# Kernel tuning notes

Measured on AMD Instinct MI355X. Metric: run time of the kernel, lower is better.

## Reference

```python
import jax, jax.numpy as jnp
import numpy as np

N_NODES = 50000
N_EDGES = 500000
D_IN = 128
D_HID = 128
C = 1.0          # curvature (same for every layer)
MIN_NORM = 1e-15
MAX_TANH_ARG = 15.0
PROJ_EPS = 4e-3  # float32 boundary eps used by hgcn PoincareBall.proj


def _artanh(x):
    x = jnp.clip(x, -1.0 + 1e-7, 1.0 - 1e-7)
    return 0.5 * (jnp.log1p(x) - jnp.log1p(-x))


def _tanh(x):
    return jnp.tanh(jnp.clip(x, -MAX_TANH_ARG, MAX_TANH_ARG))


def _norm(x):
    return jnp.maximum(jnp.linalg.norm(x, axis=-1, keepdims=True), MIN_NORM)


def proj(x, c):
    # clip points to stay strictly inside the Poincare ball
    n = _norm(x)
    maxnorm = (1.0 - PROJ_EPS) / jnp.sqrt(c)
    return jnp.where(n > maxnorm, x / n * maxnorm, x)


def expmap0(u, c):
    sc = jnp.sqrt(c)
    n = _norm(u)
    return _tanh(sc * n) * u / (sc * n)


def logmap0(p, c):
    sc = jnp.sqrt(c)
    n = _norm(p)
    return _artanh(sc * n) * p / (sc * n)


def mobius_add(x, y, c):
    x2 = jnp.sum(x * x, -1, keepdims=True)
    y2 = jnp.sum(y * y, -1, keepdims=True)
    xy = jnp.sum(x * y, -1, keepdims=True)
    num = (1.0 + 2.0 * c * xy + c * y2) * x + (1.0 - c * x2) * y
    den = 1.0 + 2.0 * c * xy + c * c * x2 * y2
    return num / jnp.maximum(den, MIN_NORM)


def mobius_matvec(m, x, c):
    sc = jnp.sqrt(c)
    xn = _norm(x)
    mx = x @ m.T                                   # [N, out]
    mxn = _norm(mx)
    res = _tanh(mxn / xn * _artanh(sc * xn)) * mx / (mxn * sc)
    is_zero = jnp.all(mx == 0.0, axis=-1, keepdims=True)
    return jnp.where(is_zero, jnp.zeros_like(res), res)


def hyp_linear(x, W, b, c):
    h = proj(mobius_matvec(W, x, c), c)
    hyp_bias = proj(expmap0(b[None, :], c), c)     # proj_tan0 is identity on the ball
    return proj(mobius_add(h, hyp_bias, c), c)


def hyp_agg(x, src, dst, edge_weight, c):
    x_tan = logmap0(x, c)                          # [N, d] tangent at origin
    msg = edge_weight[:, None] * x_tan[src]        # [E, d] gather + scale
    agg = jax.ops.segment_sum(msg, dst, num_segments=N_NODES)  # spmm(adj, x_tan)
    return proj(expmap0(agg, c), c)


def hyp_act(x, c_in, c_out):
    xt = jax.nn.relu(logmap0(x, c_in))
    return proj(expmap0(xt, c_out), c_out)


def setup_inputs() -> dict:
    key = jax.random.key(0)
    ks = jax.random.split(key, 8)
    x = jax.random.normal(ks[0], (N_NODES, D_IN), dtype=jnp.float32) * 0.1
    src = jax.random.randint(ks[1], (N_EDGES,), 0, N_NODES)
    dst = jax.random.randint(ks[2], (N_EDGES,), 0, N_NODES)
    edge_weight = jax.random.uniform(ks[3], (N_EDGES,), dtype=jnp.float32) * 0.1
    s1 = 1.0 / np.sqrt(D_IN)
    W1 = jax.random.normal(ks[4], (D_HID, D_IN), dtype=jnp.float32) * s1
    b1 = jax.random.normal(ks[5], (D_HID,), dtype=jnp.float32) * 0.01
    W2 = jax.random.normal(ks[6], (D_HID, D_HID), dtype=jnp.float32) * s1
    b2 = jax.random.normal(ks[7], (D_HID,), dtype=jnp.float32) * 0.01
    return {"x": x, "src": src, "dst": dst, "edge_weight": edge_weight,
            "W1": W1, "b1": b1, "W2": W2, "b2": b2}


def reference(x, src, dst, edge_weight, W1, b1, W2, b2):
    c = jnp.float32(C)
    # HGCN.encode: proj_tan0 (identity for PoincareBall) -> expmap0 -> proj
    h = proj(expmap0(x, c), c)
    # layer 1: HypLinear -> HypAgg -> HypAct
    h = hyp_linear(h, W1, b1, c)
    h = hyp_agg(h, src, dst, edge_weight, c)
    h = hyp_act(h, c, c)
    # layer 2
    h = hyp_linear(h, W2, b2, c)
    h = hyp_agg(h, src, dst, edge_weight, c)
    h = hyp_act(h, c, c)
    return h
```

## Files before the change

### kernel.cpp

```cpp
#include <hip/hip_runtime.h>
#include <math.h>

#define MIN_NORM 1e-15f
#define MAXNORM  0.996f
#define ARTANH_CLIP 0.99999988f

typedef __bf16 bf16x8 __attribute__((ext_vector_type(8)));
typedef float  f32x4  __attribute__((ext_vector_type(4)));

union FragU { ushort u[8]; uint4 q; bf16x8 v; };

__device__ __forceinline__ float wave_sum(float v) {
#pragma unroll
    for (int off = 32; off > 0; off >>= 1) v += __shfl_xor(v, off, 64);
    return v;
}

__device__ __forceinline__ float tanh_fast(float x) {
    const float t = __expf(2.f * fminf(x, 15.f));
    return 1.f - 2.f / (t + 1.f);
}
__device__ __forceinline__ float artanh_fast(float x) {
    x = fminf(x, ARTANH_CLIP);
    return 0.5f * __logf((1.f + x) / (1.f - x));
}

__device__ __forceinline__ float proj_factor(float n2) {
    float n = fmaxf(sqrtf(n2), MIN_NORM);
    return (n > MAXNORM) ? (MAXNORM / n) : 1.f;
}

__device__ __forceinline__ unsigned short f2bf(float f) {
    unsigned u = __float_as_uint(f);
    return (unsigned short)((u + 0x7fffu + ((u >> 16) & 1u)) >> 16);
}
__device__ __forceinline__ float bf2f(unsigned short h) {
    return __uint_as_float((unsigned)h << 16);
}
__device__ __forceinline__ float bflo(unsigned u) { return __uint_as_float(u << 16); }
__device__ __forceinline__ float bfhi(unsigned u) { return __uint_as_float(u & 0xffff0000u); }

__device__ __forceinline__ void red16_f4(float4& v) {
#pragma unroll
    for (int off = 1; off < 16; off <<= 1) {
        v.x += __shfl_xor(v.x, off, 64);
        v.y += __shfl_xor(v.y, off, 64);
        v.z += __shfl_xor(v.z, off, 64);
        v.w += __shfl_xor(v.w, off, 64);
    }
}

__device__ __forceinline__ float bcast_row(const float4& v, int r) {
    const int src = (r >> 2) << 4;
    const float a = __shfl(v.x, src, 64);
    const float b = __shfl(v.y, src, 64);
    const float c = __shfl(v.z, src, 64);
    const float d = __shfl(v.w, src, 64);
    const float lo = (r & 1) ? b : a;
    const float hi = (r & 1) ? d : c;
    return (r & 2) ? hi : lo;
}

__device__ __forceinline__ void pack_w4(const float4 w4, int o, int k, char* out) {
    ushort4 h, l;
    h.x = f2bf(w4.x); l.x = f2bf(w4.x - bf2f(h.x));
    h.y = f2bf(w4.y); l.y = f2bf(w4.y - bf2f(h.y));
    h.z = f2bf(w4.z); l.z = f2bf(w4.z - bf2f(h.z));
    h.w = f2bf(w4.w); l.w = f2bf(w4.w - bf2f(h.w));
    const int prow = ((o & 7) << 4) | (o >> 3);
    const unsigned byte = (unsigned)((prow << 8) + (k << 1)) ^ (unsigned)((prow & 7) << 4);
    *reinterpret_cast<ushort4*>(out + byte) = h;
    *reinterpret_cast<ushort4*>(out + 32768 + byte) = l;
}

__global__ void zero_cnt(int* __restrict__ cnt, int N) {
    const int i = blockIdx.x * blockDim.x + threadIdx.x;
    if (i < N) cnt[i] = 0;
}

__global__ __launch_bounds__(256)
void setup_kernel(const float* __restrict__ W1, const float* __restrict__ W2,
                  char* __restrict__ g1, char* __restrict__ g2,
                  const float* __restrict__ b1, const float* __restrict__ b2,
                  float* __restrict__ hb1, float* __restrict__ hb2,
                  const int* __restrict__ dst, int* __restrict__ cnt, int E) {
    const int b = blockIdx.x;
    if (b < 32) {
        const float* W = (b < 16) ? W1 : W2;
        char* out = (b < 16) ? g1 : g2;
        const int i = (((b & 15) * 256) + threadIdx.x) * 4;
        pack_w4(*reinterpret_cast<const float4*>(&W[i]), i >> 7, i & 127, out);
    } else if (b == 32) {
        if (threadIdx.x < 64) {
            const int lane = threadIdx.x;
#pragma unroll
            for (int j = 0; j < 2; ++j) {
                const float* bb = j ? b2 : b1;
                float* hb = j ? hb2 : hb1;
                float v0 = bb[lane], v1 = bb[lane + 64];
                float n2 = wave_sum(v0 * v0 + v1 * v1);
                float n = fmaxf(sqrtf(n2), MIN_NORM);
                float sc = tanh_fast(n) / n;
                sc *= proj_factor(sc * sc * n2);
                hb[lane] = v0 * sc;
                hb[lane + 64] = v1 * sc;
            }
        }
    } else {
        const int e = (b - 33) * 256 + threadIdx.x;
        if (e < E) atomicAdd(&cnt[dst[e]], 1);
    }
}


__global__ void scan1(const int* __restrict__ cnt, int* __restrict__ ptr,
                      int* __restrict__ bsum, int N) {
    __shared__ int s[256];
    const int t = threadIdx.x;
    const int i = blockIdx.x * 256 + t;
    int v = (i < N) ? ((cnt[i] + 3) & ~3) : 0;
    s[t] = v;
    __syncthreads();
#pragma unroll
    for (int off = 1; off < 256; off <<= 1) {
        int add = (t >= off) ? s[t - off] : 0;
        __syncthreads();
        s[t] += add;
        __syncthreads();
    }
    if (i < N) ptr[i] = s[t] - v;
    if (t == 255) bsum[blockIdx.x] = s[255];
}

__global__ void scan2(const int* __restrict__ bsum, int* __restrict__ bscan, int nb) {
    __shared__ int s[256];
    const int t = threadIdx.x;
    int v = (t < nb) ? bsum[t] : 0;
    s[t] = v;
    __syncthreads();
#pragma unroll
    for (int off = 1; off < 256; off <<= 1) {
        int add = (t >= off) ? s[t - off] : 0;
        __syncthreads();
        s[t] += add;
        __syncthreads();
    }
    bscan[t] = s[t] - v;
    if (t == 255) bscan[256] = s[255];
}

__global__ void scan3(const int* __restrict__ bscan, const int* __restrict__ cnt,
                      int* __restrict__ ptr, int* __restrict__ cursor,
                      unsigned* __restrict__ epk, int N) {
    const int i = blockIdx.x * blockDim.x + threadIdx.x;
    if (i < N) {
        const int p = ptr[i] + bscan[i >> 8];
        ptr[i] = p;
        cursor[i] = p;
        const int c = cnt[i];
        const int pc = (c + 3) & ~3;
        for (int j = c; j < pc; ++j) epk[p + j] = 0u;
    }
    if (i == 0) {
        const int tot = bscan[256];
        ptr[N] = tot;
#pragma unroll
        for (int j = 0; j < 16; ++j) epk[tot + j] = 0u;
    }
}

__global__ void scatter_kernel(const int* __restrict__ src, const int* __restrict__ dst,
                               const float* __restrict__ ew, int* __restrict__ cursor,
                               unsigned* __restrict__ epk, int E) {
    int e = blockIdx.x * blockDim.x + threadIdx.x;
    if (e >= E) return;
    int pos = atomicAdd(&cursor[dst[e]], 1);
    epk[pos] = ((unsigned)src[e] << 16) | (unsigned)f2bf(ew[e]);
}

template <bool PRELUDE, bool BF16IN, bool BF16OUT>
__global__ __launch_bounds__(512, 4)
void hyp_linear_tan_mfma(const void* __restrict__ xin, const char* __restrict__ gWpack,
                         const float* __restrict__ hb, void* __restrict__ xtan,
                         int n_rows) {
    __shared__ __align__(16) char sW[65536];

    const int tid = threadIdx.x;
    const int lane = tid & 63, wid = tid >> 6;
    const int r15 = lane & 15, g = lane >> 4;

    const int tiles = (n_rows + 15) >> 4;
    const int tile = blockIdx.x * 8 + wid;
    const bool active = (tile < tiles);
    const int rowbase = tile << 4;
    const int myrow = rowbase + r15;
    const bool rok = active && (myrow < n_rows);

    float4 xa[4], xb[4];
    uint4 xu[4];
    if (BF16IN) {
        const char* xr = (const char*)xin + (size_t)myrow * 256 + g * 16;
#pragma unroll
        for (int kc = 0; kc < 4; ++kc)
            xu[kc] = rok ? *reinterpret_cast<const uint4*>(xr + kc * 64)
                         : make_uint4(0u, 0u, 0u, 0u);
    } else {
        const float* xr = (const float*)xin + (size_t)myrow * 128 + g * 8;
#pragma unroll
        for (int kc = 0; kc < 4; ++kc) {
            if (rok) {
                xa[kc] = *reinterpret_cast<const float4*>(xr + kc * 32);
                xb[kc] = *reinterpret_cast<const float4*>(xr + kc * 32 + 4);
            } else {
                xa[kc] = make_float4(0.f, 0.f, 0.f, 0.f);
                xb[kc] = xa[kc];
            }
        }
    }

    {
        const uint4* gsrc = reinterpret_cast<const uint4*>(gWpack);
        uint4* ldst = reinterpret_cast<uint4*>(sW);
#pragma unroll
        for (int i = 0; i < 8; ++i) ldst[tid + i * 512] = gsrc[tid + i * 512];
    }

    float yb[8];
    {
        const float4 yba = *reinterpret_cast<const float4*>(&hb[r15 * 8]);
        const float4 ybb = *reinterpret_cast<const float4*>(&hb[r15 * 8 + 4]);
        yb[0] = yba.x; yb[1] = yba.y; yb[2] = yba.z; yb[3] = yba.w;
        yb[4] = ybb.x; yb[5] = ybb.y; yb[6] = ybb.z; yb[7] = ybb.w;
    }
    float y2p = 0.f;
#pragma unroll
    for (int t = 0; t < 8; ++t) y2p += yb[t] * yb[t];
#pragma unroll
    for (int off = 1; off < 16; off <<= 1) y2p += __shfl_xor(y2p, off, 64);
    const float y2 = y2p;

    __syncthreads();
    if (!active) return;

    bf16x8 ah[4], al[4];
    float ss = 0.f;
    if (BF16IN) {
#pragma unroll
        for (int kc = 0; kc < 4; ++kc) {
            FragU fu; fu.q = xu[kc];
            ah[kc] = fu.v;
            const uint4 u = xu[kc];
            float f0 = bflo(u.x), f1 = bfhi(u.x), f2_ = bflo(u.y), f3 = bfhi(u.y);
            float f4 = bflo(u.z), f5 = bfhi(u.z), f6 = bflo(u.w), f7 = bfhi(u.w);
            ss += f0 * f0 + f1 * f1 + f2_ * f2_ + f3 * f3
                + f4 * f4 + f5 * f5 + f6 * f6 + f7 * f7;
        }
    } else {
#pragma unroll
        for (int kc = 0; kc < 4; ++kc) {
            const float4 a = xa[kc], b = xb[kc];
            ss += a.x * a.x + a.y * a.y + a.z * a.z + a.w * a.w
                + b.x * b.x + b.y * b.y + b.z * b.z + b.w * b.w;
            ah[kc][0] = (__bf16)a.x; al[kc][0] = (__bf16)(a.x - (float)ah[kc][0]);
            ah[kc][1] = (__bf16)a.y; al[kc][1] = (__bf16)(a.y - (float)ah[kc][1]);
            ah[kc][2] = (__bf16)a.z; al[kc][2] = (__bf16)(a.z - (float)ah[kc][2]);
            ah[kc][3] = (__bf16)a.w; al[kc][3] = (__bf16)(a.w - (float)ah[kc][3]);
            ah[kc][4] = (__bf16)b.x; al[kc][4] = (__bf16)(b.x - (float)ah[kc][4]);
            ah[kc][5] = (__bf16)b.y; al[kc][5] = (__bf16)(b.y - (float)ah[kc][5]);
            ah[kc][6] = (__bf16)b.z; al[kc][6] = (__bf16)(b.z - (float)ah[kc][6]);
            ah[kc][7] = (__bf16)b.w; al[kc][7] = (__bf16)(b.w - (float)ah[kc][7]);
        }
    }
    ss += __shfl_xor(ss, 16, 64);
    ss += __shfl_xor(ss, 32, 64);

    f32x4 acc[8];
#pragma unroll
    for (int ct = 0; ct < 8; ++ct) acc[ct] = (f32x4){0.f, 0.f, 0.f, 0.f};

    const unsigned lswz = (unsigned)((r15 & 7) << 4);
#pragma unroll
    for (int kc = 0; kc < 4; ++kc) {
#pragma unroll
        for (int ct = 0; ct < 8; ++ct) {
            const unsigned byte =
                ((unsigned)((ct << 12) + (r15 << 8) + (kc << 6) + (g << 4))) ^ lswz;
            FragU bh, bl;
            bh.q = *reinterpret_cast<const uint4*>(sW + byte);
            bl.q = *reinterpret_cast<const uint4*>(sW + 32768 + byte);
            acc[ct] = __builtin_amdgcn_mfma_f32_16x16x32_bf16(ah[kc], bh.v, acc[ct], 0, 0, 0);
            acc[ct] = __builtin_amdgcn_mfma_f32_16x16x32_bf16(ah[kc], bl.v, acc[ct], 0, 0, 0);
            if (!BF16IN)
                acc[ct] = __builtin_amdgcn_mfma_f32_16x16x32_bf16(al[kc], bh.v, acc[ct], 0, 0, 0);
        }
    }

    float4 r2 = make_float4(0.f, 0.f, 0.f, 0.f);
    float4 xyv = make_float4(0.f, 0.f, 0.f, 0.f);
#pragma unroll
    for (int ct = 0; ct < 8; ++ct) {
        r2.x += acc[ct][0] * acc[ct][0];
        r2.y += acc[ct][1] * acc[ct][1];
        r2.z += acc[ct][2] * acc[ct][2];
        r2.w += acc[ct][3] * acc[ct][3];
        xyv.x += acc[ct][0] * yb[ct];
        xyv.y += acc[ct][1] * yb[ct];
        xyv.z += acc[ct][2] * yb[ct];
        xyv.w += acc[ct][3] * yb[ct];
    }
    red16_f4(r2);
    red16_f4(xyv);

    const float rn2 = bcast_row(r2, r15);
    const float xyr = bcast_row(xyv, r15);
    const float n2v = ss;

    const float n = fmaxf(sqrtf(n2v), MIN_NORM);
    float sc = 1.f;
    if (PRELUDE) {
        sc = tanh_fast(n) / n;
        sc *= proj_factor(sc * sc * n2v);
    }
    const float xn = fmaxf(sc * n, MIN_NORM);
    const float mxn = fmaxf(sc * sqrtf(rn2), MIN_NORM);
    const float s = tanh_fast(mxn / xn * artanh_fast(xn));
    const float sl0 = (s * sc) / mxn;
    float m2 = rn2 * sl0 * sl0;
    const float f = proj_factor(m2);
    const float scl = sl0 * f;
    m2 *= f * f;
    const float xy = scl * xyr;
    const float cx = 1.f + 2.f * xy + y2;
    const float cy = 1.f - m2;
    const float rdn = 1.f / fmaxf(1.f + 2.f * xy + m2 * y2, MIN_NORM);
    const float A = cx * scl * rdn;
    const float B = cy * rdn;
    const float on2 = A * A * rn2 + 2.f * A * B * xyr + B * B * y2;
    const float f2 = proj_factor(on2);
    const float onn = fmaxf(sqrtf(on2) * f2, MIN_NORM);
    const float slg = artanh_fast(onn) / onn;
    const float P = slg * f2 * A;
    const float Q = slg * f2 * B;

#pragma unroll
    for (int reg = 0; reg < 4; ++reg) {
        const float Pr = __shfl(P, 4 * g + reg, 64);
        const float Qr = __shfl(Q, 4 * g + reg, 64);
        const int row = rowbase + 4 * g + reg;
        if (row < n_rows) {
            float v[8];
#pragma unroll
            for (int ct = 0; ct < 8; ++ct)
                v[ct] = fmaf(Pr, acc[ct][reg], Qr * yb[ct]);
            if (BF16OUT) {
                uint4 pk;
                pk.x = (unsigned)f2bf(v[0]) | ((unsigned)f2bf(v[1]) << 16);
                pk.y = (unsigned)f2bf(v[2]) | ((unsigned)f2bf(v[3]) << 16);
                pk.z = (unsigned)f2bf(v[4]) | ((unsigned)f2bf(v[5]) << 16);
                pk.w = (unsigned)f2bf(v[6]) | ((unsigned)f2bf(v[7]) << 16);
                *reinterpret_cast<uint4*>((char*)xtan + (size_t)row * 256 + r15 * 16) = pk;
            } else {
                float* orow = (float*)xtan + (size_t)row * 128 + r15 * 8;
                *reinterpret_cast<float4*>(orow) = make_float4(v[0], v[1], v[2], v[3]);
                *reinterpret_cast<float4*>(orow + 4) = make_float4(v[4], v[5], v[6], v[7]);
            }
        }
    }
}

template <bool BF16OUT>
__global__ __launch_bounds__(256)
void gather_act(const char* __restrict__ xt, const int* __restrict__ ptr,
                const unsigned* __restrict__ epk, void* __restrict__ out, int n_rows) {
    const int v = blockIdx.x * 4 + (threadIdx.x >> 6);
    if (v >= n_rows) return;
    const int lane = threadIdx.x & 63;
    const int q = lane >> 4, t = lane & 15;
    const char* xtl = xt + (t << 4);
    const int beg = ptr[v];
    const int it = (ptr[v + 1] - beg) >> 2;

    float acc[8];
#pragma unroll
    for (int j = 0; j < 8; ++j) acc[j] = 0.f;

    const unsigned* ep = epk + beg + q;
    unsigned p = (it > 0) ? ep[0] : 0u;
    for (int k = 1; k <= it; ++k) {
        const uint4 u = *reinterpret_cast<const uint4*>(xtl + ((p >> 16) << 8));
        const unsigned pn = ep[k * 4];
        const float w = __uint_as_float(p << 16);
        acc[0] = fmaf(w, bflo(u.x), acc[0]);
        acc[1] = fmaf(w, bfhi(u.x), acc[1]);
        acc[2] = fmaf(w, bflo(u.y), acc[2]);
        acc[3] = fmaf(w, bfhi(u.y), acc[3]);
        acc[4] = fmaf(w, bflo(u.z), acc[4]);
        acc[5] = fmaf(w, bfhi(u.z), acc[5]);
        acc[6] = fmaf(w, bflo(u.w), acc[6]);
        acc[7] = fmaf(w, bfhi(u.w), acc[7]);
        p = pn;
    }

#pragma unroll
    for (int j = 0; j < 8; ++j) {
        acc[j] += __shfl_xor(acc[j], 16, 64);
        acc[j] += __shfl_xor(acc[j], 32, 64);
    }

    float s = 0.f;
#pragma unroll
    for (int j = 0; j < 8; ++j) s += acc[j] * acc[j];
#pragma unroll
    for (int off = 1; off < 16; off <<= 1) s += __shfl_xor(s, off, 64);
    const float n2 = s;

    float n = fmaxf(sqrtf(n2), MIN_NORM);
    float sc = tanh_fast(n) / n;
    float hn2 = sc * sc * n2;
    float f = proj_factor(hn2);
    sc *= f; hn2 *= f * f;
    float hn = fmaxf(sqrtf(hn2), MIN_NORM);
    float sl = artanh_fast(hn) / hn;
    const float scl1 = sc * sl;

    float x[8];
    float s2 = 0.f;
#pragma unroll
    for (int j = 0; j < 8; ++j) {
        x[j] = fmaxf(acc[j] * scl1, 0.f);
        s2 += x[j] * x[j];
    }
#pragma unroll
    for (int off = 1; off < 16; off <<= 1) s2 += __shfl_xor(s2, off, 64);
    float nb = fmaxf(sqrtf(s2), MIN_NORM);
    float scb = tanh_fast(nb) / nb;
    scb *= proj_factor(scb * scb * s2);

    const float o0 = x[2 * q] * scb, o1 = x[2 * q + 1] * scb;
    if (BF16OUT) {
        const unsigned pk = (unsigned)f2bf(o0) | ((unsigned)f2bf(o1) << 16);
        *reinterpret_cast<unsigned*>((char*)out + (size_t)v * 256 + t * 16 + q * 4) = pk;
    } else {
        *reinterpret_cast<float2*>((float*)out + (size_t)v * 128 + t * 8 + q * 2) =
            make_float2(o0, o1);
    }
}

__global__ __launch_bounds__(256)
void agg_edges(const float* __restrict__ xtan, const int* __restrict__ src,
               const int* __restrict__ dst, const float* __restrict__ ew,
               float* __restrict__ agg, int n_edges) {
    int gt = blockIdx.x * blockDim.x + threadIdx.x;
    int e = gt >> 5;
    if (e >= n_edges) return;
    int c = (gt & 31) << 2;
    int sN = src[e], dN = dst[e];
    float w = ew[e];
    const float4 v = *reinterpret_cast<const float4*>(&xtan[(size_t)sN * 128 + c]);
    float* ap = &agg[(size_t)dN * 128 + c];
    atomicAdd(ap + 0, w * v.x);
    atomicAdd(ap + 1, w * v.y);
    atomicAdd(ap + 2, w * v.z);
    atomicAdd(ap + 3, w * v.w);
}

__global__ __launch_bounds__(256)
void hyp_act_kernel(const float* __restrict__ in, float* __restrict__ out, int n_rows) {
    int row = blockIdx.x * 4 + (threadIdx.x >> 6);
    if (row >= n_rows) return;
    int lane = threadIdx.x & 63;
    int l2 = lane << 1;
    const float2 v = *reinterpret_cast<const float2*>(&in[(size_t)row * 128 + l2]);
    float a0 = v.x, a1 = v.y;
    float n2 = wave_sum(a0 * a0 + a1 * a1);
    float n = fmaxf(sqrtf(n2), MIN_NORM);
    float sc = tanh_fast(n) / n;
    float hn2 = sc * sc * n2;
    float f = proj_factor(hn2);
    sc *= f; hn2 *= f * f;
    float h0 = a0 * sc, h1 = a1 * sc;
    float hn = fmaxf(sqrtf(hn2), MIN_NORM);
    float sl = artanh_fast(hn) / hn;
    float x0 = fmaxf(h0 * sl, 0.f), x1 = fmaxf(h1 * sl, 0.f);
    float n2b = wave_sum(x0 * x0 + x1 * x1);
    float nb = fmaxf(sqrtf(n2b), MIN_NORM);
    float scb = tanh_fast(nb) / nb;
    scb *= proj_factor(scb * scb * n2b);
    *reinterpret_cast<float2*>(&out[(size_t)row * 128 + l2]) =
        make_float2(x0 * scb, x1 * scb);
}

__global__ void bias_kernel(const float* __restrict__ b1, const float* __restrict__ b2,
                            float* __restrict__ hb1, float* __restrict__ hb2) {
    int lane = threadIdx.x;
#pragma unroll
    for (int j = 0; j < 2; ++j) {
        const float* b = j ? b2 : b1;
        float* hb = j ? hb2 : hb1;
        float v0 = b[lane], v1 = b[lane + 64];
        float n2 = wave_sum(v0 * v0 + v1 * v1);
        float n = fmaxf(sqrtf(n2), MIN_NORM);
        float sc = tanh_fast(n) / n;
        sc *= proj_factor(sc * sc * n2);
        hb[lane] = v0 * sc;
        hb[lane + 64] = v1 * sc;
    }
}

__global__ void prep_w(const float* __restrict__ W1, const float* __restrict__ W2,
                       char* __restrict__ g1, char* __restrict__ g2) {
    const int b = blockIdx.x;
    const float* W = (b < 16) ? W1 : W2;
    char* out = (b < 16) ? g1 : g2;
    const int i = (((b & 15) * 256) + threadIdx.x) * 4;
    pack_w4(*reinterpret_cast<const float4*>(&W[i]), i >> 7, i & 127, out);
}

extern "C" void kernel_launch(void* const* d_in, const int* in_sizes, int n_in,
                              void* d_out, int out_size, void* d_ws, size_t ws_size,
                              hipStream_t stream) {
    const float* x   = (const float*)d_in[0];
    const int*   src = (const int*)d_in[1];
    const int*   dst = (const int*)d_in[2];
    const float* ew  = (const float*)d_in[3];
    const float* W1  = (const float*)d_in[4];
    const float* b1  = (const float*)d_in[5];
    const float* W2  = (const float*)d_in[6];
    const float* b2  = (const float*)d_in[7];

    const int N = in_sizes[0] / 128;
    const int E = in_sizes[1];
    float* fout = (float*)d_out;

    const int tiles = (N + 15) >> 4;
    const int lin_grid = (tiles + 7) / 8;
    const int nbE = (E + 255) / 256;
    const int nbN = (N + 255) / 256;

    const size_t epk_words = (size_t)E + 3 * (size_t)N + 16;

    const size_t need = 131072 + 1024
                      + (size_t)N * 256 * 2
                      + (epk_words + N) * 4
                      + ((size_t)(N + 1) + N) * 4
                      + 4096;

    if (ws_size >= need) {
        char*  base  = (char*)d_ws;
        char*  gW1p  = base;
        char*  gW2p  = base + 65536;
        float* hb1   = (float*)(base + 131072);
        float* hb2   = hb1 + 128;
        char*  xtA   = base + 131072 + 1024;
        char*  xtB   = xtA + (size_t)N * 256;
        unsigned* epk = (unsigned*)(xtB + (size_t)N * 256);
        int* cnt     = (int*)(epk + epk_words);
        int* ptr     = cnt + N;
        int* cursor  = ptr + (N + 1);
        int* bsum    = cursor + N;
        int* bscan   = bsum + 256;

        zero_cnt<<<nbN, 256, 0, stream>>>(cnt, N);
        setup_kernel<<<33 + nbE, 256, 0, stream>>>(W1, W2, gW1p, gW2p,
                                                   b1, b2, hb1, hb2, dst, cnt, E);
        scan1<<<nbN, 256, 0, stream>>>(cnt, ptr, bsum, N);
        scan2<<<1, 256, 0, stream>>>(bsum, bscan, nbN);
        scan3<<<nbN, 256, 0, stream>>>(bscan, cnt, ptr, cursor, epk, N);
        scatter_kernel<<<nbE, 256, 0, stream>>>(src, dst, ew, cursor, epk, E);

        hyp_linear_tan_mfma<true, false, true><<<lin_grid, 512, 0, stream>>>(x, gW1p, hb1, xtA, N);
        gather_act<true><<<(N + 3) / 4, 256, 0, stream>>>(xtA, ptr, epk, xtB, N);
        hyp_linear_tan_mfma<false, true, true><<<lin_grid, 512, 0, stream>>>(xtB, gW2p, hb2, xtA, N);
        gather_act<false><<<(N + 3) / 4, 256, 0, stream>>>(xtA, ptr, epk, fout, N);
    } else {
        char*  gW1p = (char*)d_ws;
        char*  gW2p = gW1p + 65536;
        float* hb1  = (float*)(gW2p + 65536);
        float* hb2  = hb1 + 128;
        float* nbuf = hb2 + 128;
        const size_t node_bytes = (size_t)N * 128 * sizeof(float);
        const int agg_blocks = (int)(((size_t)E * 32 + 255) / 256);
        const int row_blocks = (N + 3) / 4;

        prep_w<<<32, 256, 0, stream>>>(W1, W2, gW1p, gW2p);
        bias_kernel<<<1, 64, 0, stream>>>(b1, b2, hb1, hb2);
        hyp_linear_tan_mfma<true, false, false><<<lin_grid, 512, 0, stream>>>(x, gW1p, hb1, fout, N);
        hipMemsetAsync(nbuf, 0, node_bytes, stream);
        agg_edges<<<agg_blocks, 256, 0, stream>>>(fout, src, dst, ew, nbuf, E);
        hyp_act_kernel<<<row_blocks, 256, 0, stream>>>(nbuf, nbuf, N);
        hyp_linear_tan_mfma<false, false, false><<<lin_grid, 512, 0, stream>>>(nbuf, gW2p, hb2, fout, N);
        hipMemsetAsync(fout, 0, node_bytes, stream);
        agg_edges<<<agg_blocks, 256, 0, stream>>>(fout, src, dst, ew, nbuf, E);
        hyp_act_kernel<<<row_blocks, 256, 0, stream>>>(nbuf, fout, N);
    }
}
```

Measured before the change: 170.3 us.

## Split gather into feature-sliced CSR pass plus separate activation kernel

The fused gather+activation kernel is replaced by a gather_slice kernel in which each block handles one of 8 feature slices (32 bytes per row) across a grid-strided set of nodes, with 8 edges processed in parallel per wave. Its fp32 sums go to a new agg buffer, and a separate act_kernel applies expmap/proj/logmap/relu. CSR padding changes from 4 to 8, and the linear kernel's tile mapping becomes interleaved with a minimum grid of 512. The aim is better cache locality on the gathered slices (each slice of xt is small enough to stay cache-resident) at the cost of an extra fp32 round trip through memory and more launches.

```diff
diff --git a/kernel.cpp b/kernel.cpp
--- a/kernel.cpp
+++ b/kernel.cpp
@@ -118,7 +118,7 @@
     __shared__ int s[256];
     const int t = threadIdx.x;
     const int i = blockIdx.x * 256 + t;
-    int v = (i < N) ? ((cnt[i] + 3) & ~3) : 0;
+    int v = (i < N) ? ((cnt[i] + 7) & ~7) : 0;
     s[t] = v;
     __syncthreads();
 #pragma unroll
@@ -158,7 +158,7 @@
         ptr[i] = p;
         cursor[i] = p;
         const int c = cnt[i];
-        const int pc = (c + 3) & ~3;
+        const int pc = (c + 7) & ~7;
         for (int j = c; j < pc; ++j) epk[p + j] = 0u;
     }
     if (i == 0) {
@@ -182,7 +182,7 @@
 __global__ __launch_bounds__(512, 4)
 void hyp_linear_tan_mfma(const void* __restrict__ xin, const char* __restrict__ gWpack,
                          const float* __restrict__ hb, void* __restrict__ xtan,
-                         int n_rows) {
+                         int n_rows, int ngrid) {
     __shared__ __align__(16) char sW[65536];
 
     const int tid = threadIdx.x;
@@ -190,7 +190,7 @@
     const int r15 = lane & 15, g = lane >> 4;
 
     const int tiles = (n_rows + 15) >> 4;
-    const int tile = blockIdx.x * 8 + wid;
+    const int tile = blockIdx.x + ngrid * wid;
     const bool active = (tile < tiles);
     const int rowbase = tile << 4;
     const int myrow = rowbase + r15;
@@ -368,52 +368,49 @@
     }
 }
 
+__global__ __launch_bounds__(256)
+void gather_slice(const char* __restrict__ xt, const int* __restrict__ ptr,
+                  const unsigned* __restrict__ epk, float* __restrict__ agg,
+                  int n_rows, int ngrp) {
+    const int s = blockIdx.x & 7;
+    const int lane = threadIdx.x & 63;
+    const int e8 = lane >> 3, c = lane & 7;
+    const char* xts = xt + s * 32 + c * 4;
+
+    for (int v = (blockIdx.x >> 3) * 4 + ((int)threadIdx.x >> 6); v < n_rows; v += ngrp * 4) {
+        const int beg = ptr[v];
+        const int it = (ptr[v + 1] - beg) >> 3;
+
+        float a0 = 0.f, a1 = 0.f;
+        const unsigned* ep = epk + beg + e8;
+        unsigned p = (it > 0) ? ep[0] : 0u;
+        for (int k = 1; k <= it; ++k) {
+            const unsigned u = *reinterpret_cast<const unsigned*>(xts + ((p >> 16) << 8));
+            const unsigned pn = ep[k * 8];
+            const float w = __uint_as_float(p << 16);
+            a0 = fmaf(w, bflo(u), a0);
+            a1 = fmaf(w, bfhi(u), a1);
+            p = pn;
+        }
+        a0 += __shfl_xor(a0, 8, 64);  a1 += __shfl_xor(a1, 8, 64);
+        a0 += __shfl_xor(a0, 16, 64); a1 += __shfl_xor(a1, 16, 64);
+        a0 += __shfl_xor(a0, 32, 64); a1 += __shfl_xor(a1, 32, 64);
+        if (e8 == 0)
+            *reinterpret_cast<float2*>(agg + (size_t)v * 128 + s * 16 + c * 2) =
+                make_float2(a0, a1);
+    }
+}
+
 template <bool BF16OUT>
-__global__ __launch_bounds__(256)
-void gather_act(const char* __restrict__ xt, const int* __restrict__ ptr,
-                const unsigned* __restrict__ epk, void* __restrict__ out, int n_rows) {
-    const int v = blockIdx.x * 4 + (threadIdx.x >> 6);
+__global__ __launch_bounds__(1024)
+void act_kernel(const float* __restrict__ agg, void* __restrict__ out, int n_rows) {
+    const int v = blockIdx.x * 16 + ((int)threadIdx.x >> 6);
     if (v >= n_rows) return;
-    const int lane = threadIdx.x & 63;
-    const int q = lane >> 4, t = lane & 15;
-    const char* xtl = xt + (t << 4);
-    const int beg = ptr[v];
-    const int it = (ptr[v + 1] - beg) >> 2;
-
-    float acc[8];
-#pragma unroll
-    for (int j = 0; j < 8; ++j) acc[j] = 0.f;
-
-    const unsigned* ep = epk + beg + q;
-    unsigned p = (it > 0) ? ep[0] : 0u;
-    for (int k = 1; k <= it; ++k) {
-        const uint4 u = *reinterpret_cast<const uint4*>(xtl + ((p >> 16) << 8));
-        const unsigned pn = ep[k * 4];
-        const float w = __uint_as_float(p << 16);
-        acc[0] = fmaf(w, bflo(u.x), acc[0]);
-        acc[1] = fmaf(w, bfhi(u.x), acc[1]);
-        acc[2] = fmaf(w, bflo(u.y), acc[2]);
-        acc[3] = fmaf(w, bfhi(u.y), acc[3]);
-        acc[4] = fmaf(w, bflo(u.z), acc[4]);
-        acc[5] = fmaf(w, bfhi(u.z), acc[5]);
-        acc[6] = fmaf(w, bflo(u.w), acc[6]);
-        acc[7] = fmaf(w, bfhi(u.w), acc[7]);
-        p = pn;
-    }
-
-#pragma unroll
-    for (int j = 0; j < 8; ++j) {
-        acc[j] += __shfl_xor(acc[j], 16, 64);
-        acc[j] += __shfl_xor(acc[j], 32, 64);
-    }
-
-    float s = 0.f;
-#pragma unroll
-    for (int j = 0; j < 8; ++j) s += acc[j] * acc[j];
-#pragma unroll
-    for (int off = 1; off < 16; off <<= 1) s += __shfl_xor(s, off, 64);
-    const float n2 = s;
-
+    const int lane = threadIdx.x & 63, l2 = lane << 1;
+    const float2 a = *reinterpret_cast<const float2*>(agg + (size_t)v * 128 + l2);
+    float a0 = a.x, a1 = a.y;
+
+    float n2 = wave_sum(a0 * a0 + a1 * a1);
     float n = fmaxf(sqrtf(n2), MIN_NORM);
     float sc = tanh_fast(n) / n;
     float hn2 = sc * sc * n2;
@@ -422,26 +419,18 @@
     float hn = fmaxf(sqrtf(hn2), MIN_NORM);
     float sl = artanh_fast(hn) / hn;
     const float scl1 = sc * sl;
-
-    float x[8];
-    float s2 = 0.f;
-#pragma unroll
-    for (int j = 0; j < 8; ++j) {
-        x[j] = fmaxf(acc[j] * scl1, 0.f);
-        s2 += x[j] * x[j];
-    }
-#pragma unroll
-    for (int off = 1; off < 16; off <<= 1) s2 += __shfl_xor(s2, off, 64);
-    float nb = fmaxf(sqrtf(s2), MIN_NORM);
+    float x0 = fmaxf(a0 * scl1, 0.f), x1 = fmaxf(a1 * scl1, 0.f);
+    float n2b = wave_sum(x0 * x0 + x1 * x1);
+    float nb = fmaxf(sqrtf(n2b), MIN_NORM);
     float scb = tanh_fast(nb) / nb;
-    scb *= proj_factor(scb * scb * s2);
-
-    const float o0 = x[2 * q] * scb, o1 = x[2 * q + 1] * scb;
+    scb *= proj_factor(scb * scb * n2b);
+    const float o0 = x0 * scb, o1 = x1 * scb;
+
     if (BF16OUT) {
         const unsigned pk = (unsigned)f2bf(o0) | ((unsigned)f2bf(o1) << 16);
-        *reinterpret_cast<unsigned*>((char*)out + (size_t)v * 256 + t * 16 + q * 4) = pk;
+        *reinterpret_cast<unsigned*>((char*)out + (size_t)v * 256 + lane * 4) = pk;
     } else {
-        *reinterpret_cast<float2*>((float*)out + (size_t)v * 128 + t * 8 + q * 2) =
+        *reinterpret_cast<float2*>((float*)out + (size_t)v * 128 + l2) =
             make_float2(o0, o1);
     }
 }
@@ -533,14 +522,19 @@
     float* fout = (float*)d_out;
 
     const int tiles = (N + 15) >> 4;
-    const int lin_grid = (tiles + 7) / 8;
+    int lin_grid = (tiles + 7) / 8;
+    if (lin_grid < 512) lin_grid = 512;
     const int nbE = (E + 255) / 256;
     const int nbN = (N + 255) / 256;
-
-    const size_t epk_words = (size_t)E + 3 * (size_t)N + 16;
+    const int act_grid = (N + 15) / 16;
+    const int gs_grp = 512;
+    const int gs_grid = gs_grp * 8;
+
+    const size_t epk_words = (size_t)E + 7 * (size_t)N + 16;
 
     const size_t need = 131072 + 1024
                       + (size_t)N * 256 * 2
+                      + (size_t)N * 512
                       + (epk_words + N) * 4
                       + ((size_t)(N + 1) + N) * 4
                       + 4096;
@@ -553,7 +547,8 @@
         float* hb2   = hb1 + 128;
         char*  xtA   = base + 131072 + 1024;
         char*  xtB   = xtA + (size_t)N * 256;
-        unsigned* epk = (unsigned*)(xtB + (size_t)N * 256);
+        float* agg   = (float*)(xtB + (size_t)N * 256);
+        unsigned* epk = (unsigned*)(agg + (size_t)N * 128);
         int* cnt     = (int*)(epk + epk_words);
         int* ptr     = cnt + N;
         int* cursor  = ptr + (N + 1);
@@ -566,12 +561,16 @@
         scan1<<<nbN, 256, 0, stream>>>(cnt, ptr, bsum, N);
         scan2<<<1, 256, 0, stream>>>(bsum, bscan, nbN);
         scan3<<<nbN, 256, 0, stream>>>(bscan, cnt, ptr, cursor, epk, N);
-        scatter_kernel<<<nbE, 256, 0, stream>>>(src, dst, ew, cursor, epk, E);
-
-        hyp_linear_tan_mfma<true, false, true><<<lin_grid, 512, 0, stream>>>(x, gW1p, hb1, xtA, N);
-        gather_act<true><<<(N + 3) / 4, 256, 0, stream>>>(xtA, ptr, epk, xtB, N);
-        hyp_linear_tan_mfma<false, true, true><<<lin_grid, 512, 0, stream>>>(xtB, gW2p, hb2, xtA, N);
-        gather_act<false><<<(N + 3) / 4, 256, 0, stream>>>(xtA, ptr, epk, fout, N);
+        scatter_kernel<<<(E + 511) / 512, 512, 0, stream>>>(src, dst, ew, cursor, epk, E);
+
+        hyp_linear_tan_mfma<true, false, true><<<lin_grid, 512, 0, stream>>>(
+            x, gW1p, hb1, xtA, N, lin_grid);
+        gather_slice<<<gs_grid, 256, 0, stream>>>(xtA, ptr, epk, agg, N, gs_grp);
+        act_kernel<true><<<act_grid, 1024, 0, stream>>>(agg, xtB, N);
+        hyp_linear_tan_mfma<false, true, true><<<lin_grid, 512, 0, stream>>>(
+            xtB, gW2p, hb2, xtA, N, lin_grid);
+        gather_slice<<<gs_grid, 256, 0, stream>>>(xtA, ptr, epk, agg, N, gs_grp);
+        act_kernel<false><<<act_grid, 1024, 0, stream>>>(agg, fout, N);
     } else {
         char*  gW1p = (char*)d_ws;
         char*  gW2p = gW1p + 65536;
@@ -584,11 +583,13 @@
 
         prep_w<<<32, 256, 0, stream>>>(W1, W2, gW1p, gW2p);
         bias_kernel<<<1, 64, 0, stream>>>(b1, b2, hb1, hb2);
-        hyp_linear_tan_mfma<true, false, false><<<lin_grid, 512, 0, stream>>>(x, gW1p, hb1, fout, N);
+        hyp_linear_tan_mfma<true, false, false><<<lin_grid, 512, 0, stream>>>(
+            x, gW1p, hb1, fout, N, lin_grid);
         hipMemsetAsync(nbuf, 0, node_bytes, stream);
         agg_edges<<<agg_blocks, 256, 0, stream>>>(fout, src, dst, ew, nbuf, E);
         hyp_act_kernel<<<row_blocks, 256, 0, stream>>>(nbuf, nbuf, N);
-        hyp_linear_tan_mfma<false, false, false><<<lin_grid, 512, 0, stream>>>(nbuf, gW2p, hb2, fout, N);
+        hyp_linear_tan_mfma<false, false, false><<<lin_grid, 512, 0, stream>>>(
+            nbuf, gW2p, hb2, fout, N, lin_grid);
         hipMemsetAsync(fout, 0, node_bytes, stream);
         agg_edges<<<agg_blocks, 256, 0, stream>>>(fout, src, dst, ew, nbuf, E);
         hyp_act_kernel<<<row_blocks, 256, 0, stream>>>(nbuf, fout, N);
```

Result: slower. 288.9 us (+69.7%).
